# Kernel optimization log

Measured on AMD Instinct MI355X. Metric: run time of the kernel, lower is better.

The kernel has to match this reference:

```python
import jax, jax.numpy as jnp
import numpy as np

EPS = 1e-8


def _pairwise_cosine(x, y):
    # F.cosine_similarity clamps each norm to eps before dividing.
    xn = x / jnp.maximum(jnp.linalg.norm(x, axis=-1, keepdims=True), EPS)
    yn = y / jnp.maximum(jnp.linalg.norm(y, axis=-1, keepdims=True), EPS)
    # torch layout: sim[i, j] = cos(y[i], x[j]) -> [N, N]
    return jnp.einsum('id,jd->ij', yn, xn)


def _kl_loss(target_logits, predicted_logits):
    t = jax.nn.softmax(target_logits, axis=-1)
    log_t = jax.nn.log_softmax(target_logits, axis=-1)
    log_p = jax.nn.log_softmax(predicted_logits, axis=-1)
    kl = jnp.sum(t * (log_t - log_p), axis=-1)
    return jnp.mean(kl)


def setup_inputs() -> dict:
    key = jax.random.key(0)
    k1, k2 = jax.random.split(key)
    N, D = 4096, 1024
    target = jax.random.normal(k1, (N, D), dtype=jnp.float32)
    predicted = jax.random.normal(k2, (N, D), dtype=jnp.float32)
    return {"target": target, "predicted": predicted}


def reference(target, predicted):
    x1 = _pairwise_cosine(target, target)      # [N, N]
    x2 = _pairwise_cosine(predicted, predicted)
    return _kl_loss(x1, x2) + _kl_loss(target, predicted)
```

## Files before the change

### kernel.cpp

```cpp
#include <hip/hip_runtime.h>
#include <hip/hip_bf16.h>
#include <math.h>

#define N 4096
#define D 1024
#define PANEL 128
#define NPANEL 32
#define NTRI (NPANEL * (NPANEL + 1) / 2)
#define BK 32
#define NITER (D / BK)
#define PANBYTES 131072

typedef float f32x4 __attribute__((ext_vector_type(4)));


__global__ void zero_kernel(float* p) {
  int i = blockIdx.x * 256 + threadIdx.x;
  if (i < N * 3) p[i] = 0.0f;
}

__global__ __launch_bounds__(256) void prep_kernel(const float* __restrict__ tgt,
                                                   const float* __restrict__ prd,
                                                   uint8_t* __restrict__ tn,
                                                   uint8_t* __restrict__ pn,
                                                   float* __restrict__ rowkl) {
  const int wid = threadIdx.x >> 6, lane = threadIdx.x & 63;
  const int row = blockIdx.x * 4 + wid;
  const float* tr = tgt + (size_t)row * D;
  const float* pr = prd + (size_t)row * D;
  float4 tv[4], pv[4];
  #pragma unroll
  for (int j = 0; j < 4; j++) {
    tv[j] = ((const float4*)tr)[j * 64 + lane];
    pv[j] = ((const float4*)pr)[j * 64 + lane];
  }
  float ss_t = 0.f, ss_p = 0.f, mx_t = -1e30f, mx_p = -1e30f;
  #pragma unroll
  for (int j = 0; j < 4; j++) {
    float t_[4] = {tv[j].x, tv[j].y, tv[j].z, tv[j].w};
    float p_[4] = {pv[j].x, pv[j].y, pv[j].z, pv[j].w};
    #pragma unroll
    for (int k = 0; k < 4; k++) {
      ss_t += t_[k] * t_[k]; ss_p += p_[k] * p_[k];
      mx_t = fmaxf(mx_t, t_[k]); mx_p = fmaxf(mx_p, p_[k]);
    }
  }
  #pragma unroll
  for (int o = 32; o > 0; o >>= 1) {
    ss_t += __shfl_xor(ss_t, o);
    ss_p += __shfl_xor(ss_p, o);
    mx_t = fmaxf(mx_t, __shfl_xor(mx_t, o));
    mx_p = fmaxf(mx_p, __shfl_xor(mx_p, o));
  }
  float rnt = 1.0f / fmaxf(sqrtf(ss_t), 1e-8f);
  float rnp = 1.0f / fmaxf(sqrtf(ss_p), 1e-8f);

  const int P = row >> 7, r = row & 127;
  const int kcsub = lane >> 3;
  const int G = (lane & 7) >> 1;
  const int Gs = G ^ ((r >> 2) & 3);
  const int bphys = (Gs << 3) | ((lane & 1) * 4);

  float et = 0.f, ep = 0.f, sv = 0.f;
  #pragma unroll
  for (int j = 0; j < 4; j++) {
    float t_[4] = {tv[j].x, tv[j].y, tv[j].z, tv[j].w};
    float p_[4] = {pv[j].x, pv[j].y, pv[j].z, pv[j].w};
    uint32_t tpack = 0, ppack = 0;
    tpack = __builtin_amdgcn_cvt_pk_fp8_f32(t_[0] * rnt, t_[1] * rnt, tpack, false);
    tpack = __builtin_amdgcn_cvt_pk_fp8_f32(t_[2] * rnt, t_[3] * rnt, tpack, true);
    ppack = __builtin_amdgcn_cvt_pk_fp8_f32(p_[0] * rnp, p_[1] * rnp, ppack, false);
    ppack = __builtin_amdgcn_cvt_pk_fp8_f32(p_[2] * rnp, p_[3] * rnp, ppack, true);
    size_t off = ((size_t)(P * 32 + j * 8 + kcsub)) * 4096 + r * 32 + bphys;
    *(uint32_t*)(tn + off) = tpack;
    *(uint32_t*)(pn + off) = ppack;
    #pragma unroll
    for (int k = 0; k < 4; k++) {
      float e = __expf(t_[k] - mx_t);
      et += e; sv += e * (t_[k] - p_[k]);
      ep += __expf(p_[k] - mx_p);
    }
  }
  #pragma unroll
  for (int o = 32; o > 0; o >>= 1) {
    et += __shfl_xor(et, o);
    ep += __shfl_xor(ep, o);
    sv += __shfl_xor(sv, o);
  }
  if (lane == 0)
    rowkl[row] = sv / et - (mx_t - mx_p + __logf(et) - __logf(ep));
}

__global__ __launch_bounds__(256, 2) void gram_kernel(const uint8_t* __restrict__ tn,
                                                      const uint8_t* __restrict__ pn,
                                                      float* __restrict__ rowstats) {
  __shared__ __align__(16) uint8_t smem[4 * 16384];
  const int tid = threadIdx.x;
  const int wid = tid >> 6, lane = tid & 63;
  const int g = lane >> 4, lr = lane & 15;
  const int wr = wid >> 1, wc = wid & 1;

  int p = (blockIdx.x & 7) * (NTRI / 8) + (blockIdx.x >> 3);
  int rem = p, R = 0, C = 0;
  bool found = false;
  for (R = 0; R < 4 && !found; R++) {
    for (C = R; C < 4; C++) {
      int sz = (R == C) ? 36 : 64;
      if (rem < sz) { found = true; break; }
      rem -= sz;
    }
  }
  R--;
  int pr, pc;
  if (R == C) {
    pr = 0;
    while (rem >= 8 - pr) { rem -= 8 - pr; pr++; }
    pc = pr + rem;
  } else {
    pr = rem >> 3; pc = rem & 7;
  }
  const int rb = R * 8 + pr, cc = C * 8 + pc;
  const int rowbase = rb * PANEL, colbase = cc * PANEL;

  const uint8_t* mats[2] = {tn, pn};
  const uint8_t* srcp[4];
  #pragma unroll
  for (int i = 0; i < 4; i++) {
    int isB = i >> 1, mat = i & 1;
    srcp[i] = mats[mat] + (size_t)(isB ? cc : rb) * PANBYTES + tid * 16;
  }
  auto stage = [&](int buf, int k) {
    #pragma unroll
    for (int i = 0; i < 4; i++)
      __builtin_amdgcn_global_load_lds(
          (const __attribute__((address_space(1))) void*)(srcp[i] + k * 4096),
          (__attribute__((address_space(3))) void*)(smem + buf * 16384 + i * 4096 + tid * 16),
          16, 0, 0);
  };

  f32x4 acc[4][4][2];
  #pragma unroll
  for (int rt = 0; rt < 4; rt++)
    #pragma unroll
    for (int ct = 0; ct < 4; ct++)
      #pragma unroll
      for (int m = 0; m < 2; m++)
        acc[rt][ct][m] = (f32x4){0.f, 0.f, 0.f, 0.f};

  auto body = [&](int buf) {
    const uint8_t* sa = smem + buf * 16384;
    long a[4][2];
    #pragma unroll
    for (int rt = 0; rt < 4; rt++) {
      int row = wr * 64 + rt * 16 + lr;
      int sw = (row >> 2) & 3;
      #pragma unroll
      for (int m = 0; m < 2; m++)
        a[rt][m] = *(const long*)(sa + m * 4096 + row * 32 + ((g ^ sw) << 3));
    }
    #pragma unroll
    for (int ct = 0; ct < 4; ct++) {
      int col = wc * 64 + ct * 16 + lr;
      int sw = (col >> 2) & 3;
      #pragma unroll
      for (int m = 0; m < 2; m++) {
        long b = *(const long*)(sa + 8192 + m * 4096 + col * 32 + ((g ^ sw) << 3));
        #pragma unroll
        for (int rt = 0; rt < 4; rt++)
          acc[rt][ct][m] =
              __builtin_amdgcn_mfma_f32_16x16x32_fp8_fp8(a[rt][m], b, acc[rt][ct][m], 0, 0, 0);
      }
    }
  };

  stage(0, 0); stage(1, 1); stage(2, 2);

  for (int k = 0; k < NITER - 2; k++) {
    asm volatile("s_waitcnt vmcnt(8)" ::: "memory");
    __builtin_amdgcn_s_barrier();
    if (k + 3 < NITER) stage((k + 3) & 3, k + 3);
    body(k & 3);
  }
  asm volatile("s_waitcnt vmcnt(4)" ::: "memory");
  __builtin_amdgcn_s_barrier();
  body((NITER - 2) & 3);
  asm volatile("s_waitcnt vmcnt(0)" ::: "memory");
  __builtin_amdgcn_s_barrier();
  body((NITER - 1) & 3);

  #pragma unroll
  for (int rt = 0; rt < 4; rt++) {
    #pragma unroll
    for (int r = 0; r < 4; r++) {
      float e1 = 0.f, e2 = 0.f, sl = 0.f;
      #pragma unroll
      for (int ct = 0; ct < 4; ct++) {
        float s1 = acc[rt][ct][0][r], s2 = acc[rt][ct][1][r];
        float pw = __expf(s1 - 1.0f);
        e1 += pw; sl += pw * (s1 - s2);
        e2 += __expf(s2 - 1.0f);
      }
      #pragma unroll
      for (int mk = 1; mk < 16; mk <<= 1) {
        e1 += __shfl_xor(e1, mk);
        e2 += __shfl_xor(e2, mk);
        sl += __shfl_xor(sl, mk);
      }
      if (lr == 0) {
        int row = rowbase + wr * 64 + rt * 16 + g * 4 + r;
        atomicAdd(&rowstats[row * 3 + 0], e1);
        atomicAdd(&rowstats[row * 3 + 1], e2);
        atomicAdd(&rowstats[row * 3 + 2], sl);
      }
    }
  }
  if (rb != cc) {
    #pragma unroll
    for (int ct = 0; ct < 4; ct++) {
      float e1 = 0.f, e2 = 0.f, sl = 0.f;
      #pragma unroll
      for (int rt = 0; rt < 4; rt++)
        #pragma unroll
        for (int r = 0; r < 4; r++) {
          float s1 = acc[rt][ct][0][r], s2 = acc[rt][ct][1][r];
          float pw = __expf(s1 - 1.0f);
          e1 += pw; sl += pw * (s1 - s2);
          e2 += __expf(s2 - 1.0f);
        }
      e1 += __shfl_xor(e1, 16); e2 += __shfl_xor(e2, 16); sl += __shfl_xor(sl, 16);
      e1 += __shfl_xor(e1, 32); e2 += __shfl_xor(e2, 32); sl += __shfl_xor(sl, 32);
      if (g == 0) {
        int col = colbase + wc * 64 + ct * 16 + lr;
        atomicAdd(&rowstats[col * 3 + 0], e1);
        atomicAdd(&rowstats[col * 3 + 1], e2);
        atomicAdd(&rowstats[col * 3 + 2], sl);
      }
    }
  }
}

__global__ __launch_bounds__(1024) void finalize_kernel(const float* __restrict__ rowstats,
                                                        const float* __restrict__ rowkl,
                                                        float* __restrict__ out) {
  __shared__ float buf[16];
  float s = 0.f;
  for (int r = threadIdx.x; r < N; r += 1024) {
    float e1 = rowstats[r * 3 + 0];
    float e2 = rowstats[r * 3 + 1];
    float sl = rowstats[r * 3 + 2];
    s += sl / e1 - (__logf(e1) - __logf(e2)) + rowkl[r];
  }
  #pragma unroll
  for (int o = 32; o > 0; o >>= 1) s += __shfl_xor(s, o);
  if ((threadIdx.x & 63) == 0) buf[threadIdx.x >> 6] = s;
  __syncthreads();
  if (threadIdx.x == 0) {
    float t = 0.f;
    #pragma unroll
    for (int i = 0; i < 16; i++) t += buf[i];
    out[0] = t * (1.0f / (float)N);
  }
}

extern "C" void kernel_launch(void* const* d_in, const int* in_sizes, int n_in,
                              void* d_out, int out_size, void* d_ws, size_t ws_size,
                              hipStream_t stream) {
  const float* tgt = (const float*)d_in[0];
  const float* prd = (const float*)d_in[1];
  float* out = (float*)d_out;
  char* ws = (char*)d_ws;
  uint8_t* tn = (uint8_t*)ws;
  uint8_t* pn = (uint8_t*)(ws + 4194304);
  float* rowstats = (float*)(ws + 8388608);
  float* rowkl = rowstats + N * 3;

  zero_kernel<<<(N * 3 + 255) / 256, 256, 0, stream>>>(rowstats);
  prep_kernel<<<N / 4, 256, 0, stream>>>(tgt, prd, tn, pn, rowkl);
  gram_kernel<<<NTRI, 256, 0, stream>>>(tn, pn, rowstats);
  finalize_kernel<<<1, 1024, 0, stream>>>(rowstats, rowkl, out);
}
```

Measured before the change: 99.58 us.

## Load fp8 MFMA operands directly from global into registers, dropping LDS staging

Measured after the change: 105.9 us. +6.3%, slower.

```diff
diff --git a/kernel.cpp b/kernel.cpp
--- a/kernel.cpp
+++ b/kernel.cpp
@@ -94,7 +94,6 @@
 __global__ __launch_bounds__(256, 2) void gram_kernel(const uint8_t* __restrict__ tn,
                                                       const uint8_t* __restrict__ pn,
                                                       float* __restrict__ rowstats) {
-  __shared__ __align__(16) uint8_t smem[4 * 16384];
   const int tid = threadIdx.x;
   const int wid = tid >> 6, lane = tid & 63;
   const int g = lane >> 4, lr = lane & 15;
@@ -122,21 +121,14 @@
   const int rb = R * 8 + pr, cc = C * 8 + pc;
   const int rowbase = rb * PANEL, colbase = cc * PANEL;
 
-  const uint8_t* mats[2] = {tn, pn};
-  const uint8_t* srcp[4];
-  #pragma unroll
-  for (int i = 0; i < 4; i++) {
-    int isB = i >> 1, mat = i & 1;
-    srcp[i] = mats[mat] + (size_t)(isB ? cc : rb) * PANBYTES + tid * 16;
-  }
-  auto stage = [&](int buf, int k) {
-    #pragma unroll
-    for (int i = 0; i < 4; i++)
-      __builtin_amdgcn_global_load_lds(
-          (const __attribute__((address_space(1))) void*)(srcp[i] + k * 4096),
-          (__attribute__((address_space(3))) void*)(smem + buf * 16384 + i * 4096 + tid * 16),
-          16, 0, 0);
-  };
+  const uint32_t sw = (lr >> 2) & 3;
+  const uint32_t fo = (uint32_t)lr * 32 + ((g ^ sw) << 3);
+  const uint32_t offA = (uint32_t)wr * 2048 + fo;
+  const uint32_t offB = (uint32_t)wc * 2048 + fo;
+  const uint8_t* baseA0 = tn + (size_t)rb * PANBYTES + offA;
+  const uint8_t* baseA1 = pn + (size_t)rb * PANBYTES + offA;
+  const uint8_t* baseB0 = tn + (size_t)cc * PANBYTES + offB;
+  const uint8_t* baseB1 = pn + (size_t)cc * PANBYTES + offB;
 
   f32x4 acc[4][4][2];
   #pragma unroll
@@ -147,46 +139,42 @@
       for (int m = 0; m < 2; m++)
         acc[rt][ct][m] = (f32x4){0.f, 0.f, 0.f, 0.f};
 
-  auto body = [&](int buf) {
-    const uint8_t* sa = smem + buf * 16384;
-    long a[4][2];
-    #pragma unroll
-    for (int rt = 0; rt < 4; rt++) {
-      int row = wr * 64 + rt * 16 + lr;
-      int sw = (row >> 2) & 3;
-      #pragma unroll
-      for (int m = 0; m < 2; m++)
-        a[rt][m] = *(const long*)(sa + m * 4096 + row * 32 + ((g ^ sw) << 3));
-    }
-    #pragma unroll
-    for (int ct = 0; ct < 4; ct++) {
-      int col = wc * 64 + ct * 16 + lr;
-      int sw = (col >> 2) & 3;
-      #pragma unroll
-      for (int m = 0; m < 2; m++) {
-        long b = *(const long*)(sa + 8192 + m * 4096 + col * 32 + ((g ^ sw) << 3));
-        #pragma unroll
-        for (int rt = 0; rt < 4; rt++)
-          acc[rt][ct][m] =
-              __builtin_amdgcn_mfma_f32_16x16x32_fp8_fp8(a[rt][m], b, acc[rt][ct][m], 0, 0, 0);
-      }
-    }
-  };
-
-  stage(0, 0); stage(1, 1); stage(2, 2);
-
-  for (int k = 0; k < NITER - 2; k++) {
-    asm volatile("s_waitcnt vmcnt(8)" ::: "memory");
-    __builtin_amdgcn_s_barrier();
-    if (k + 3 < NITER) stage((k + 3) & 3, k + 3);
-    body(k & 3);
-  }
-  asm volatile("s_waitcnt vmcnt(4)" ::: "memory");
-  __builtin_amdgcn_s_barrier();
-  body((NITER - 2) & 3);
-  asm volatile("s_waitcnt vmcnt(0)" ::: "memory");
-  __builtin_amdgcn_s_barrier();
-  body((NITER - 1) & 3);
+  long a0[4][2], b0[4][2], a1[4][2], b1[4][2];
+
+#define LOADSET(aS, bS, kc)                                                \
+  {                                                                        \
+    const uint32_t ko = (uint32_t)(kc) * 4096;                             \
+    _Pragma("unroll")                                                      \
+    for (int rt = 0; rt < 4; rt++) {                                       \
+      aS[rt][0] = *(const long*)(baseA0 + ko + rt * 512);                  \
+      aS[rt][1] = *(const long*)(baseA1 + ko + rt * 512);                  \
+    }                                                                      \
+    _Pragma("unroll")                                                      \
+    for (int ct = 0; ct < 4; ct++) {                                       \
+      bS[ct][0] = *(const long*)(baseB0 + ko + ct * 512);                  \
+      bS[ct][1] = *(const long*)(baseB1 + ko + ct * 512);                  \
+    }                                                                      \
+  }
+
+#define BODYSET(aS, bS)                                                    \
+  _Pragma("unroll")                                                        \
+  for (int ct = 0; ct < 4; ct++)                                           \
+    _Pragma("unroll")                                                      \
+    for (int m = 0; m < 2; m++)                                            \
+      _Pragma("unroll")                                                    \
+      for (int rt = 0; rt < 4; rt++)                                       \
+        acc[rt][ct][m] = __builtin_amdgcn_mfma_f32_16x16x32_fp8_fp8(       \
+            aS[rt][m], bS[ct][m], acc[rt][ct][m], 0, 0, 0);
+
+  LOADSET(a0, b0, 0);
+  for (int k = 0; k < NITER; k += 2) {
+    LOADSET(a1, b1, k + 1);
+    BODYSET(a0, b0);
+    if (k + 2 < NITER) LOADSET(a0, b0, k + 2);
+    BODYSET(a1, b1);
+  }
+#undef LOADSET
+#undef BODYSET
 
   #pragma unroll
   for (int rt = 0; rt < 4; rt++) {
```
